# Performance work log

Measured on AMD Instinct MI355X. Metric: run time of the kernel, lower is better.

The kernel has to match this reference:

```python
import jax, jax.numpy as jnp
import numpy as np

N = 100000        # nodes
E = 1_600_000     # edges (avg degree 16)
IN = 128          # in_feats
HID = 64          # hidden_feats
H = 3             # num_heads
OUT = 16          # out_feats
NEG_SLOPE = 0.2   # DGL GATConv default LeakyReLU slope


def setup_inputs() -> dict:
    key = jax.random.key(0)
    ks = jax.random.split(key, 16)
    f = lambda k, shape, s=0.1: (jax.random.normal(k, shape, jnp.float32) * s)
    return {
        "features": f(ks[0], (N, IN), 1.0),
        "src": jax.random.randint(ks[1], (E,), 0, N),
        "dst": jax.random.randint(ks[2], (E,), 0, N),
        # GATConv 1: in -> (H, HID)
        "W1": f(ks[3], (IN, H * HID)),
        "al1": f(ks[4], (H, HID)),
        "ar1": f(ks[5], (H, HID)),
        "b1": f(ks[6], (H, HID)),
        # GATConv 2: H*HID -> (H, HID)
        "W2": f(ks[7], (H * HID, H * HID)),
        "al2": f(ks[8], (H, HID)),
        "ar2": f(ks[9], (H, HID)),
        "b2": f(ks[10], (H, HID)),
        # MLP head
        "w3": f(ks[11], (H * HID, HID)),
        "b3": f(ks[12], (HID,)),
        "w4": f(ks[13], (HID, OUT)),
        "b4": f(ks[14], (OUT,)),
    }


def gat_layer(x, src, dst, W, al, ar, b):
    # feat: (N, H, D) projected features
    feat = (x @ W).reshape(-1, H, HID)
    el = jnp.einsum('nhd,hd->nh', feat, al)   # (N, H)
    er = jnp.einsum('nhd,hd->nh', feat, ar)   # (N, H)
    e = el[src] + er[dst]                     # (E, H) edge scores
    e = jnp.where(e > 0, e, NEG_SLOPE * e)    # LeakyReLU
    # numerically stable softmax over incoming edges of each dst node
    m = jax.lax.stop_gradient(jax.ops.segment_max(e, dst, num_segments=N))
    ex = jnp.exp(e - m[dst])
    s = jax.ops.segment_sum(ex, dst, num_segments=N)
    alpha = ex / s[dst]                       # (E, H)
    # message passing: scatter alpha-weighted src features to dst
    out = jax.ops.segment_sum(alpha[:, :, None] * feat[src], dst, num_segments=N)
    return jax.nn.relu(out + b)               # (N, H, D)


def reference(features, src, dst, W1, al1, ar1, b1, W2, al2, ar2, b2, w3, b3, w4, b4):
    x = gat_layer(features, src, dst, W1, al1, ar1, b1).reshape(N, H * HID)
    x = gat_layer(x, src, dst, W2, al2, ar2, b2).reshape(N, H * HID)
    h = jax.nn.relu(x @ w3 + b3)
    return h @ w4 + b4
```

## Files before the change

### kernel.cpp

```cpp
#include <hip/hip_runtime.h>
#include <cstdint>
#include <cstddef>

#define NN   100000
#define EE   1600000
#define INF_ 128
#define HIDF 64
#define NH   3
#define FEAT 192
#define OUTF 16
#define NEG  0.2f

#define NI4  25000
#define NB   98

typedef unsigned short ushort_t;
typedef unsigned int   uint_t;

__device__ __forceinline__ float bf2f(ushort_t u) {
    return __uint_as_float(((uint_t)u) << 16);
}
__device__ __forceinline__ ushort_t f2bf(float f) {
    uint_t b = __float_as_uint(f);
    return (ushort_t)((b + 0x7FFFu + ((b >> 16) & 1u)) >> 16);
}


__global__ void hist_kernel(const int* __restrict__ dst, int* __restrict__ counts) {
    int e = blockIdx.x * 256 + threadIdx.x;
    if (e < EE) atomicAdd(&counts[dst[e]], 1);
}

__global__ __launch_bounds__(256) void blocksum_kernel(const int* __restrict__ counts,
                                                       int* __restrict__ bsum) {
    int t = threadIdx.x;
    int idx4 = blockIdx.x * 256 + t;
    int s = 0;
    if (idx4 < NI4) {
        int4 v = ((const int4*)counts)[idx4];
        s = v.x + v.y + v.z + v.w;
    }
    __shared__ int sd[4];
    for (int o = 32; o; o >>= 1) s += __shfl_down(s, o, 64);
    if ((t & 63) == 0) sd[t >> 6] = s;
    __syncthreads();
    if (t == 0) bsum[blockIdx.x] = sd[0] + sd[1] + sd[2] + sd[3];
}

__global__ __launch_bounds__(128) void scanb_kernel(int* __restrict__ bsum) {
    __shared__ int sd[128];
    int t = threadIdx.x;
    int v = (t < NB) ? bsum[t] : 0;
    sd[t] = v;
    __syncthreads();
    for (int o = 1; o < 128; o <<= 1) {
        int u = (t >= o) ? sd[t - o] : 0;
        __syncthreads();
        sd[t] += u;
        __syncthreads();
    }
    if (t < NB) bsum[t] = sd[t] - v;
}

__global__ __launch_bounds__(256) void scanfinal_kernel(const int* __restrict__ counts,
                                                        const int* __restrict__ bsum,
                                                        int* __restrict__ row_ptr,
                                                        int* __restrict__ cursor) {
    __shared__ int sd[256];
    int t = threadIdx.x;
    int idx4 = blockIdx.x * 256 + t;
    int4 v = make_int4(0, 0, 0, 0);
    if (idx4 < NI4) v = ((const int4*)counts)[idx4];
    int s = v.x + v.y + v.z + v.w;
    sd[t] = s;
    __syncthreads();
    for (int o = 1; o < 256; o <<= 1) {
        int u = (t >= o) ? sd[t - o] : 0;
        __syncthreads();
        sd[t] += u;
        __syncthreads();
    }
    int base = bsum[blockIdx.x] + sd[t] - s;
    if (idx4 < NI4) {
        int4 r;
        r.x = base;
        r.y = base + v.x;
        r.z = base + v.x + v.y;
        r.w = base + v.x + v.y + v.z;
        ((int4*)row_ptr)[idx4] = r;
        ((int4*)cursor)[idx4]  = r;
    }
    if (blockIdx.x == 0 && t == 0) row_ptr[NN] = EE;
}

__global__ void scatter_kernel(const int* __restrict__ src, const int* __restrict__ dst,
                               int* __restrict__ cursor, int* __restrict__ ssrc) {
    int e = blockIdx.x * 256 + threadIdx.x;
    if (e < EE) {
        int p = atomicAdd(&cursor[dst[e]], 1);
        ssrc[p] = src[e];
    }
}


template <int K, int N, bool BIAS, bool RELU, bool ELER, bool A_BF16, bool C_BF16>
__global__ __launch_bounds__(256) void gemm64_kernel(const void* __restrict__ Av,
                                                     const float* __restrict__ B,
                                                     const float* __restrict__ bias,
                                                     void* __restrict__ Cv,
                                                     const float* __restrict__ al,
                                                     const float* __restrict__ ar,
                                                     float* __restrict__ el,
                                                     float* __restrict__ er) {
    __shared__ float As[32][64];
    __shared__ float Bs[32][64];
    const int m0 = blockIdx.x * 64;
    const int n0 = blockIdx.y * 64;
    const int t  = threadIdx.x;
    const int tr = t >> 4;
    const int tc = t & 15;

    float acc[4][4] = {};

    for (int kt = 0; kt < K; kt += 32) {
        if (A_BF16) {
            const ushort_t* A = (const ushort_t*)Av;
            int row = t >> 2, c8 = (t & 3) * 8;
            int gr = m0 + row;
            if (gr < NN) {
                uint4 v = *(const uint4*)(A + (size_t)gr * K + kt + c8);
                As[c8 + 0][row] = bf2f((ushort_t)(v.x & 0xffff));
                As[c8 + 1][row] = bf2f((ushort_t)(v.x >> 16));
                As[c8 + 2][row] = bf2f((ushort_t)(v.y & 0xffff));
                As[c8 + 3][row] = bf2f((ushort_t)(v.y >> 16));
                As[c8 + 4][row] = bf2f((ushort_t)(v.z & 0xffff));
                As[c8 + 5][row] = bf2f((ushort_t)(v.z >> 16));
                As[c8 + 6][row] = bf2f((ushort_t)(v.w & 0xffff));
                As[c8 + 7][row] = bf2f((ushort_t)(v.w >> 16));
            } else {
#pragma unroll
                for (int j = 0; j < 8; ++j) As[c8 + j][row] = 0.f;
            }
        } else {
            const float* A = (const float*)Av;
            int f = t;
#pragma unroll
            for (int it = 0; it < 2; ++it, f += 256) {
                int row = f >> 3, c4 = (f & 7) * 4;
                float4 v = make_float4(0.f, 0.f, 0.f, 0.f);
                int gr = m0 + row;
                if (gr < NN) v = *(const float4*)(A + (size_t)gr * K + kt + c4);
                As[c4 + 0][row] = v.x;
                As[c4 + 1][row] = v.y;
                As[c4 + 2][row] = v.z;
                As[c4 + 3][row] = v.w;
            }
        }
        {
            int f = t;
#pragma unroll
            for (int it = 0; it < 2; ++it, f += 256) {
                int row = f >> 4, c4 = (f & 15) * 4;
                *(float4*)&Bs[row][c4] = *(const float4*)(B + (size_t)(kt + row) * N + n0 + c4);
            }
        }
        __syncthreads();
#pragma unroll
        for (int k = 0; k < 32; ++k) {
            float4 a = *(const float4*)&As[k][tr * 4];
            float4 b = *(const float4*)&Bs[k][tc * 4];
            acc[0][0] += a.x * b.x; acc[0][1] += a.x * b.y; acc[0][2] += a.x * b.z; acc[0][3] += a.x * b.w;
            acc[1][0] += a.y * b.x; acc[1][1] += a.y * b.y; acc[1][2] += a.y * b.z; acc[1][3] += a.y * b.w;
            acc[2][0] += a.z * b.x; acc[2][1] += a.z * b.y; acc[2][2] += a.z * b.z; acc[2][3] += a.z * b.w;
            acc[3][0] += a.w * b.x; acc[3][1] += a.w * b.y; acc[3][2] += a.w * b.z; acc[3][3] += a.w * b.w;
        }
        __syncthreads();
    }

    float4 bv = make_float4(0.f, 0.f, 0.f, 0.f);
    if (BIAS) bv = *(const float4*)(bias + n0 + tc * 4);
#pragma unroll
    for (int i = 0; i < 4; ++i) {
        int row = m0 + tr * 4 + i;
        if (row >= NN) continue;
        float4 r;
        r.x = acc[i][0]; r.y = acc[i][1]; r.z = acc[i][2]; r.w = acc[i][3];
        if (BIAS) { r.x += bv.x; r.y += bv.y; r.z += bv.z; r.w += bv.w; }
        if (RELU) {
            r.x = fmaxf(r.x, 0.f); r.y = fmaxf(r.y, 0.f);
            r.z = fmaxf(r.z, 0.f); r.w = fmaxf(r.w, 0.f);
        }
        if (C_BF16) {
            ushort4 u;
            u.x = f2bf(r.x); u.y = f2bf(r.y); u.z = f2bf(r.z); u.w = f2bf(r.w);
            *(ushort4*)((ushort_t*)Cv + (size_t)row * N + n0 + tc * 4) = u;
        } else {
            *(float4*)((float*)Cv + (size_t)row * N + n0 + tc * 4) = r;
        }
    }

    if (ELER) {
        const int h = blockIdx.y;
        float4 va = *(const float4*)(al + h * HIDF + tc * 4);
        float4 vb = *(const float4*)(ar + h * HIDF + tc * 4);
#pragma unroll
        for (int i = 0; i < 4; ++i) {
            float pl = acc[i][0] * va.x + acc[i][1] * va.y + acc[i][2] * va.z + acc[i][3] * va.w;
            float pr = acc[i][0] * vb.x + acc[i][1] * vb.y + acc[i][2] * vb.z + acc[i][3] * vb.w;
#pragma unroll
            for (int o = 1; o < 16; o <<= 1) {
                pl += __shfl_xor(pl, o, 16);
                pr += __shfl_xor(pr, o, 16);
            }
            int row = m0 + tr * 4 + i;
            if (tc == 0 && row < NN) {
                el[row * NH + h] = pl;
                er[row * NH + h] = pr;
            }
        }
    }
}


template <int K, int M, int ROWS, bool BIAS, bool RELU>
__global__ void rowgemm_kernel(const float* __restrict__ A, const float* __restrict__ W,
                               const float* __restrict__ bias, float* __restrict__ C) {
    __shared__ float a[ROWS][K];
    const int BT = M * ROWS;
    int r0 = blockIdx.x * ROWS;
    for (int i = threadIdx.x; i < ROWS * K; i += BT) {
        int rr = i / K, kk = i - rr * K;
        int row = r0 + rr;
        a[rr][kk] = (row < NN) ? A[(size_t)row * K + kk] : 0.f;
    }
    __syncthreads();
    int rr = threadIdx.x / M, c = threadIdx.x - rr * M;
    int row = r0 + rr;
    if (row >= NN) return;
    float acc = 0.f;
#pragma unroll
    for (int k = 0; k < K; ++k) acc += a[rr][k] * W[k * M + c];
    if (BIAS) acc += bias[c];
    if (RELU) acc = fmaxf(acc, 0.f);
    C[(size_t)row * M + c] = acc;
}


__global__ __launch_bounds__(256) void aggregate_kernel(
    const int* __restrict__ row_ptr, const int* __restrict__ ssrc,
    const ushort_t* __restrict__ featb, const float* __restrict__ el,
    const float* __restrict__ er, const float* __restrict__ bias,
    ushort_t* __restrict__ outb) {
    int w = blockIdx.x * 4 + (threadIdx.x >> 6);
    if (w >= NN) return;
    int lane = threadIdx.x & 63;
    int beg = row_ptr[w], end = row_ptr[w + 1];
    float er0 = er[w * 3 + 0], er1 = er[w * 3 + 1], er2 = er[w * 3 + 2];

    float s0 = 0.f, s1 = 0.f, s2 = 0.f;
    float acc0 = 0.f, acc1 = 0.f, acc2 = 0.f;
    for (int e = beg; e < end; ++e) {
        int s = ssrc[e];
        float a0 = el[s * 3 + 0] + er0; a0 = a0 > 0.f ? a0 : NEG * a0;
        float a1 = el[s * 3 + 1] + er1; a1 = a1 > 0.f ? a1 : NEG * a1;
        float a2 = el[s * 3 + 2] + er2; a2 = a2 > 0.f ? a2 : NEG * a2;
        float w0 = __expf(a0), w1 = __expf(a1), w2 = __expf(a2);
        s0 += w0; s1 += w1; s2 += w2;
        const ushort_t* fr = featb + (size_t)s * FEAT;
        acc0 += w0 * bf2f(fr[lane]);
        acc1 += w1 * bf2f(fr[64 + lane]);
        acc2 += w2 * bf2f(fr[128 + lane]);
    }

    float r0, r1, r2;
    if (end > beg) { r0 = acc0 / s0; r1 = acc1 / s1; r2 = acc2 / s2; }
    else           { r0 = r1 = r2 = 0.f; }
    r0 += bias[lane]; r1 += bias[64 + lane]; r2 += bias[128 + lane];
    outb[(size_t)w * FEAT + lane]       = f2bf(fmaxf(r0, 0.f));
    outb[(size_t)w * FEAT + 64 + lane]  = f2bf(fmaxf(r1, 0.f));
    outb[(size_t)w * FEAT + 128 + lane] = f2bf(fmaxf(r2, 0.f));
}


extern "C" void kernel_launch(void* const* d_in, const int* in_sizes, int n_in,
                              void* d_out, int out_size, void* d_ws, size_t ws_size,
                              hipStream_t stream) {
    const float* features = (const float*)d_in[0];
    const int*   src      = (const int*)d_in[1];
    const int*   dst      = (const int*)d_in[2];
    const float* W1  = (const float*)d_in[3];
    const float* al1 = (const float*)d_in[4];
    const float* ar1 = (const float*)d_in[5];
    const float* b1  = (const float*)d_in[6];
    const float* W2  = (const float*)d_in[7];
    const float* al2 = (const float*)d_in[8];
    const float* ar2 = (const float*)d_in[9];
    const float* b2  = (const float*)d_in[10];
    const float* w3  = (const float*)d_in[11];
    const float* b3  = (const float*)d_in[12];
    const float* w4  = (const float*)d_in[13];
    const float* b4  = (const float*)d_in[14];
    float* out = (float*)d_out;

    char* p = (char*)d_ws;
    ushort_t* featb = (ushort_t*)p; p += (size_t)NN * FEAT * 2;
    ushort_t* xb    = (ushort_t*)p; p += (size_t)NN * FEAT * 2;
    float* hid = (float*)p; p += (size_t)NN * HIDF * 4;
    float* el  = (float*)p; p += (size_t)NN * NH * 4;
    float* er  = (float*)p; p += (size_t)NN * NH * 4;
    int* counts  = (int*)p;  p += (size_t)NN * 4;
    int* row_ptr = (int*)p;  p += (size_t)(NN + 4) * 4;
    int* cursor  = (int*)p;  p += (size_t)NN * 4;
    int* ssrc    = (int*)p;  p += (size_t)EE * 4;
    int* bsum    = (int*)p;  p += 128 * 4;

    const int GM = (NN + 63) / 64;

    hipMemsetAsync(counts, 0, (size_t)NN * 4, stream);
    hist_kernel<<<(EE + 255) / 256, 256, 0, stream>>>(dst, counts);
    blocksum_kernel<<<NB, 256, 0, stream>>>(counts, bsum);
    scanb_kernel<<<1, 128, 0, stream>>>(bsum);
    scanfinal_kernel<<<NB, 256, 0, stream>>>(counts, bsum, row_ptr, cursor);
    scatter_kernel<<<(EE + 255) / 256, 256, 0, stream>>>(src, dst, cursor, ssrc);

    gemm64_kernel<INF_, FEAT, false, false, true, false, true>
        <<<dim3(GM, FEAT / 64), 256, 0, stream>>>(features, W1, nullptr, featb, al1, ar1, el, er);
    aggregate_kernel<<<(NN + 3) / 4, 256, 0, stream>>>(row_ptr, ssrc, featb, el, er, b1, xb);

    gemm64_kernel<FEAT, FEAT, false, false, true, true, true>
        <<<dim3(GM, FEAT / 64), 256, 0, stream>>>(xb, W2, nullptr, featb, al2, ar2, el, er);
    aggregate_kernel<<<(NN + 3) / 4, 256, 0, stream>>>(row_ptr, ssrc, featb, el, er, b2, xb);

    gemm64_kernel<FEAT, HIDF, true, true, false, true, false>
        <<<dim3(GM, 1), 256, 0, stream>>>(xb, w3, b3, hid, nullptr, nullptr, nullptr, nullptr);
    rowgemm_kernel<HIDF, OUTF, 16, true, false><<<NN / 16, 256, 0, stream>>>(hid, w4, b4, out);
}
```

Measured before the change: 907.9 us.

## Precompute per-edge attention weights in a separate edge-parallel kernel

Splits the edge-score computation (LeakyReLU plus exp of el[src]+er[dst]) out of the per-node aggregation loop into an edge-parallel kernel that writes a weight array, using a new sorted dst array produced by the scatter. The aggregation loop then reads precomputed weights and marks the source index wave-uniform via readfirstlane. This is meant to take the dependent gathers and exp work off the serial per-node critical loop and parallelise them across edges. The cost is an extra kernel launch per layer plus writing and re-reading about 19 MB of weights and 6.4 MB of sdst. The weight buffer reuses the hid scratch space.

```diff
diff --git a/kernel.cpp b/kernel.cpp
--- a/kernel.cpp
+++ b/kernel.cpp
@@ -94,12 +94,32 @@
 }
 
 __global__ void scatter_kernel(const int* __restrict__ src, const int* __restrict__ dst,
-                               int* __restrict__ cursor, int* __restrict__ ssrc) {
+                               int* __restrict__ cursor, int* __restrict__ ssrc,
+                               int* __restrict__ sdst) {
     int e = blockIdx.x * 256 + threadIdx.x;
     if (e < EE) {
-        int p = atomicAdd(&cursor[dst[e]], 1);
+        int d = dst[e];
+        int p = atomicAdd(&cursor[d], 1);
         ssrc[p] = src[e];
-    }
+        sdst[p] = d;
+    }
+}
+
+
+__global__ __launch_bounds__(256) void edgew_kernel(const int* __restrict__ ssrc,
+                                                    const int* __restrict__ sdst,
+                                                    const float* __restrict__ el,
+                                                    const float* __restrict__ er,
+                                                    float* __restrict__ wgt) {
+    int p = blockIdx.x * 256 + threadIdx.x;
+    if (p >= EE) return;
+    int s = ssrc[p], d = sdst[p];
+    float a0 = el[s * 3 + 0] + er[d * 3 + 0]; a0 = a0 > 0.f ? a0 : NEG * a0;
+    float a1 = el[s * 3 + 1] + er[d * 3 + 1]; a1 = a1 > 0.f ? a1 : NEG * a1;
+    float a2 = el[s * 3 + 2] + er[d * 3 + 2]; a2 = a2 > 0.f ? a2 : NEG * a2;
+    wgt[p * 3 + 0] = __expf(a0);
+    wgt[p * 3 + 1] = __expf(a1);
+    wgt[p * 3 + 2] = __expf(a2);
 }
 
 
@@ -248,23 +268,21 @@
 
 __global__ __launch_bounds__(256) void aggregate_kernel(
     const int* __restrict__ row_ptr, const int* __restrict__ ssrc,
-    const ushort_t* __restrict__ featb, const float* __restrict__ el,
-    const float* __restrict__ er, const float* __restrict__ bias,
+    const float* __restrict__ wgt,
+    const ushort_t* __restrict__ featb, const float* __restrict__ bias,
     ushort_t* __restrict__ outb) {
     int w = blockIdx.x * 4 + (threadIdx.x >> 6);
     if (w >= NN) return;
     int lane = threadIdx.x & 63;
     int beg = row_ptr[w], end = row_ptr[w + 1];
-    float er0 = er[w * 3 + 0], er1 = er[w * 3 + 1], er2 = er[w * 3 + 2];
 
     float s0 = 0.f, s1 = 0.f, s2 = 0.f;
     float acc0 = 0.f, acc1 = 0.f, acc2 = 0.f;
-    for (int e = beg; e < end; ++e) {
-        int s = ssrc[e];
-        float a0 = el[s * 3 + 0] + er0; a0 = a0 > 0.f ? a0 : NEG * a0;
-        float a1 = el[s * 3 + 1] + er1; a1 = a1 > 0.f ? a1 : NEG * a1;
-        float a2 = el[s * 3 + 2] + er2; a2 = a2 > 0.f ? a2 : NEG * a2;
-        float w0 = __expf(a0), w1 = __expf(a1), w2 = __expf(a2);
+    for (int p = beg; p < end; ++p) {
+        int s = __builtin_amdgcn_readfirstlane(ssrc[p]);
+        float w0 = wgt[p * 3 + 0];
+        float w1 = wgt[p * 3 + 1];
+        float w2 = wgt[p * 3 + 2];
         s0 += w0; s1 += w1; s2 += w2;
         const ushort_t* fr = featb + (size_t)s * FEAT;
         acc0 += w0 * bf2f(fr[lane]);
@@ -305,31 +323,38 @@
     char* p = (char*)d_ws;
     ushort_t* featb = (ushort_t*)p; p += (size_t)NN * FEAT * 2;
     ushort_t* xb    = (ushort_t*)p; p += (size_t)NN * FEAT * 2;
-    float* hid = (float*)p; p += (size_t)NN * HIDF * 4;
+    float* scratch  = (float*)p;    p += (size_t)NN * HIDF * 4;
     float* el  = (float*)p; p += (size_t)NN * NH * 4;
     float* er  = (float*)p; p += (size_t)NN * NH * 4;
     int* counts  = (int*)p;  p += (size_t)NN * 4;
     int* row_ptr = (int*)p;  p += (size_t)(NN + 4) * 4;
     int* cursor  = (int*)p;  p += (size_t)NN * 4;
     int* ssrc    = (int*)p;  p += (size_t)EE * 4;
+    int* sdst    = (int*)p;  p += (size_t)EE * 4;
     int* bsum    = (int*)p;  p += 128 * 4;
 
+    float* wgt = scratch;
+    float* hid = scratch;
+
     const int GM = (NN + 63) / 64;
+    const int GE = (EE + 255) / 256;
 
     hipMemsetAsync(counts, 0, (size_t)NN * 4, stream);
-    hist_kernel<<<(EE + 255) / 256, 256, 0, stream>>>(dst, counts);
+    hist_kernel<<<GE, 256, 0, stream>>>(dst, counts);
     blocksum_kernel<<<NB, 256, 0, stream>>>(counts, bsum);
     scanb_kernel<<<1, 128, 0, stream>>>(bsum);
     scanfinal_kernel<<<NB, 256, 0, stream>>>(counts, bsum, row_ptr, cursor);
-    scatter_kernel<<<(EE + 255) / 256, 256, 0, stream>>>(src, dst, cursor, ssrc);
+    scatter_kernel<<<GE, 256, 0, stream>>>(src, dst, cursor, ssrc, sdst);
 
     gemm64_kernel<INF_, FEAT, false, false, true, false, true>
         <<<dim3(GM, FEAT / 64), 256, 0, stream>>>(features, W1, nullptr, featb, al1, ar1, el, er);
-    aggregate_kernel<<<(NN + 3) / 4, 256, 0, stream>>>(row_ptr, ssrc, featb, el, er, b1, xb);
+    edgew_kernel<<<GE, 256, 0, stream>>>(ssrc, sdst, el, er, wgt);
+    aggregate_kernel<<<(NN + 3) / 4, 256, 0, stream>>>(row_ptr, ssrc, wgt, featb, b1, xb);
 
     gemm64_kernel<FEAT, FEAT, false, false, true, true, true>
         <<<dim3(GM, FEAT / 64), 256, 0, stream>>>(xb, W2, nullptr, featb, al2, ar2, el, er);
-    aggregate_kernel<<<(NN + 3) / 4, 256, 0, stream>>>(row_ptr, ssrc, featb, el, er, b2, xb);
+    edgew_kernel<<<GE, 256, 0, stream>>>(ssrc, sdst, el, er, wgt);
+    aggregate_kernel<<<(NN + 3) / 4, 256, 0, stream>>>(row_ptr, ssrc, wgt, featb, b2, xb);
 
     gemm64_kernel<FEAT, HIDF, true, true, false, true, false>
         <<<dim3(GM, 1), 256, 0, stream>>>(xb, w3, b3, hid, nullptr, nullptr, nullptr, nullptr);
```

New measurement: 889.5 us. -2.0%, faster.
